# Performance work log

Hardware: AMD Instinct MI355X
Metric: run time of the kernel (lower is better)

## Reference

```python
import jax, jax.numpy as jnp
import numpy as np
from jax import lax

C, NORI, NROT, K, PAD = 256, 8, 2, 3, 1
B, H, W = 16, 64, 64
EPS = 1e-5


def setup_inputs() -> dict:
    key = jax.random.key(0)
    k1, k2, k3 = jax.random.split(key, 3)
    x = jax.random.normal(k1, (B, C, H, W), dtype=jnp.float32)
    # rotate_arf() output: [nRot*C, nOri*C, K, K]
    weight_all = jax.random.normal(k2, (NROT * C, NORI * C, K, K), dtype=jnp.float32) * 0.02
    bias_all = jax.random.normal(k3, (NROT * C,), dtype=jnp.float32) * 0.02
    alpha = jnp.float32(1.0)
    gamma = jnp.ones((C,), dtype=jnp.float32)
    beta = jnp.zeros((C,), dtype=jnp.float32)
    return {"x": x, "weight_all": weight_all, "bias_all": bias_all,
            "alpha": alpha, "gamma": gamma, "beta": beta}


def _forward(x, weight_all, bias_all, alpha, gamma, beta):
    # Loop of nOri*nRot convs over the same x with different weight blocks,
    # all accumulated into one [B,C,H,W] tensor == single conv with summed blocks
    # (conv is linear in the weights): fused form of the original loop.
    W_eff = weight_all.reshape(NROT, C, NORI, C, K, K).sum(axis=(0, 2))  # [C, C, K, K]
    b_eff = bias_all.reshape(NROT, C).sum(axis=0) * NORI                 # [C]
    d_sum = lax.conv_general_dilated(
        x, W_eff, window_strides=(1, 1), padding=[(PAD, PAD), (PAD, PAD)],
        dimension_numbers=("NCHW", "OIHW", "NCHW"))
    d_sum = d_sum + b_eff[None, :, None, None]
    d_mean = d_sum / float(NORI * NROT)
    out = x + alpha * d_mean
    # BatchNorm2d, training mode: biased batch stats over (B, H, W)
    mean = out.mean(axis=(0, 2, 3))
    var = ((out - mean[None, :, None, None]) ** 2).mean(axis=(0, 2, 3))
    inv = lax.rsqrt(var + EPS)
    y = (out - mean[None, :, None, None]) * (gamma * inv)[None, :, None, None] \
        + beta[None, :, None, None]
    return y


def reference(x, weight_all, bias_all, alpha, gamma, beta):
    return _forward(x, weight_all, bias_all, alpha, gamma, beta)
```

## Files before the change

kernel.cpp:

```cpp
#include <hip/hip_runtime.h>
#include <stdint.h>

typedef __attribute__((__ext_vector_type__(8))) __bf16 bf16x8;
typedef __attribute__((__ext_vector_type__(4))) float  f32x4;

#define XT_OFF    0ul
#define WT_OFF    33554432ul
#define BEFF_OFF  34734080ul
#define ZERO_OFF  34737152ul
#define STATS_OFF 34737408ul

__device__ inline void gload_lds16(const void* g, void* l) {
  __builtin_amdgcn_global_load_lds((const __attribute__((address_space(1))) void*)g,
                                   (__attribute__((address_space(3))) void*)l,
                                   16, 0, 0);
}

__global__ void k_wred(const float* __restrict__ w, const float* __restrict__ bias,
                       const float* __restrict__ alpha_p, __bf16* __restrict__ Wt,
                       float* __restrict__ beff, float* __restrict__ zerob,
                       float* __restrict__ statsG) {
  const int co = blockIdx.x;
  const int ci = threadIdx.x;
  float a[9];
#pragma unroll
  for (int t = 0; t < 9; ++t) a[t] = 0.f;
#pragma unroll
  for (int r = 0; r < 2; ++r)
#pragma unroll
    for (int o = 0; o < 8; ++o) {
      const float* p = w + ((size_t)(r * 256 + co) * 2048 + (size_t)(o * 256 + ci)) * 9;
#pragma unroll
      for (int t = 0; t < 9; ++t) a[t] += p[t];
    }
  const float sc = alpha_p[0] * 0.0625f;
#pragma unroll
  for (int t = 0; t < 9; ++t)
    Wt[((size_t)co * 9 + t) * 256 + ci] = (__bf16)(a[t] * sc);
  if (ci == 0) beff[co] = (bias[co] + bias[256 + co]) * 8.0f * sc;
  if (blockIdx.x == 0) {
    statsG[ci] = 0.f; statsG[256 + ci] = 0.f;
    if (ci < 64) zerob[ci] = 0.f;
  }
}

__global__ void k_xpose(const float* __restrict__ x, __bf16* __restrict__ xT) {
  __shared__ __bf16 lds[64 * 258];
  int bh = blockIdx.x;
  int b = bh >> 6, h = bh & 63;
  int t = threadIdx.x;
  int w = t & 63, cg = t >> 6;
  const float* xb = x + ((size_t)b * 16384 + h) * 64;
#pragma unroll 4
  for (int cb = 0; cb < 256; cb += 4) {
    int ci = cb + cg;
    lds[w * 258 + ci] = (__bf16)xb[(size_t)ci * 4096 + w];
  }
  __syncthreads();
  const uint32_t* l32 = (const uint32_t*)lds;
  uint32_t* o32 = (uint32_t*)(xT + ((size_t)b * 64 + h) * 64 * 256);
  int c2 = t & 127, wg = t >> 7;
  for (int w0 = 0; w0 < 64; w0 += 2) {
    int ww = w0 + wg;
    o32[ww * 128 + c2] = l32[ww * 129 + c2];
  }
}

#define A_BYTES 51200
#define B_BYTES 32768

__global__ __launch_bounds__(1024) void k_conv(
    const float* __restrict__ x, const __bf16* __restrict__ xT,
    const __bf16* __restrict__ Wt, const float* __restrict__ beff,
    const __bf16* __restrict__ zerob, float* __restrict__ out,
    float* __restrict__ statsG)
{
  __shared__ __align__(16) char lds[A_BYTES + 2 * B_BYTES];
  const int bb   = blockIdx.x >> 4;
  const int ho0  = (blockIdx.x & 15) << 2;
  const int tid  = threadIdx.x;
  const int lane = tid & 63;
  const int wid  = tid >> 6;
  const int wr   = wid >> 2;
  const int wc   = wid & 3;

  f32x4 acc[4][4];
#pragma unroll
  for (int i = 0; i < 4; ++i)
#pragma unroll
    for (int j = 0; j < 4; ++j)
#pragma unroll
      for (int r = 0; r < 4; ++r) acc[i][j][r] = 0.f;

  const char* zb = (const char*)zerob;

  int boff[4][2];
#pragma unroll
  for (int j = 0; j < 4; ++j)
#pragma unroll
    for (int kk = 0; kk < 2; ++kk) {
      const int co     = (wc << 6) + (j << 4) + (lane & 15);
      const int ci_off = (kk << 5) + ((lane >> 4) << 3);
      boff[j][kk] = ((co << 7) + (ci_off << 1)) ^ ((co & 7) << 4);
    }
  const int bl = lane >> 3;
  const size_t bsrcLane = (size_t)bl * 4608 + (size_t)(((lane & 7) ^ (bl & 7)) << 4);

  auto stageA = [&](int s) {
    const int ci0 = s << 6;
    for (int t = wid; t < 50; t += 16) {
      const int ch = (t << 3) + (lane >> 3);
      const int r  = ch / 66;
      const int c  = ch - r * 66;
      const int ir = ho0 - 1 + r;
      const int ic = c - 1;
      const int k  = (lane & 7) ^ (ch & 7);
      const char* src;
      if (ch < 396 && ir >= 0 && ir < 64 && ic >= 0 && ic < 64)
        src = (const char*)(xT + ((((size_t)bb << 6) + ir) * 64 + ic) * 256 + ci0 + (k << 3));
      else
        src = zb + (k << 4);
      gload_lds16(src, lds + (t << 10));
    }
  };

  auto stageB = [&](int bi, int phOff ) {
    char* buf = lds + A_BYTES + bi * B_BYTES;
    const char* wsrc = (const char*)Wt + bsrcLane + phOff;
    gload_lds16(wsrc + (size_t)wid * 36864, buf + (wid << 10));
    gload_lds16(wsrc + (size_t)(wid + 16) * 36864, buf + ((wid + 16) << 10));
  };

  stageA(0);
  stageB(0, 0);
  __syncthreads();

  int pb = 0;
  for (int s = 0; s < 4; ++s) {
    for (int tap = 0; tap < 9; ++tap) {
      const int p = s * 9 + tap;
      if (p + 1 < 36) {
        int ntap = tap + 1, ns = s;
        if (ntap == 9) { ntap = 0; ++ns; }
        stageB(pb ^ 1, ((ntap << 8) + (ns << 6)) << 1);
      }
      const int dh = (tap >= 6) ? 2 : (tap >= 3 ? 1 : 0);
      const int dw = tap - dh * 3;
      const char* Bb = lds + A_BYTES + pb * B_BYTES;
      __builtin_amdgcn_s_setprio(1);
#pragma unroll
      for (int kk = 0; kk < 2; ++kk) {
        const int ci_off = (kk << 5) + ((lane >> 4) << 3);
        bf16x8 av[4];
#pragma unroll
        for (int i = 0; i < 4; ++i) {
          const int pos = (wr + dh) * 66 + (i << 4) + (lane & 15) + dw;
          const int off = ((pos << 7) + (ci_off << 1)) ^ ((pos & 7) << 4);
          av[i] = *(const bf16x8*)(lds + off);
        }
#pragma unroll
        for (int j = 0; j < 4; ++j) {
          const bf16x8 bv = *(const bf16x8*)(Bb + boff[j][kk]);
#pragma unroll
          for (int i = 0; i < 4; ++i)
            acc[i][j] = __builtin_amdgcn_mfma_f32_16x16x32_bf16(av[i], bv, acc[i][j], 0, 0, 0);
        }
      }
      __builtin_amdgcn_s_setprio(0);
      __syncthreads();
      if (tap == 8 && s < 3) {
        stageA(s + 1);
        __syncthreads();
      }
      pb ^= 1;
    }
  }

  __syncthreads();
  float* sw    = (float*)lds + wid * 1040;
  float* lstat = (float*)(lds + 112640);
  if (tid < 512) lstat[tid] = 0.f;
  __syncthreads();

  const int cl = lane & 15, ch4 = (lane >> 4) << 2;
  const int ho = ho0 + wr;
  const int cc2 = lane >> 2, q = lane & 3;
#pragma unroll
  for (int j = 0; j < 4; ++j) {
    asm volatile("s_waitcnt lgkmcnt(0)" ::: "memory");
#pragma unroll
    for (int i = 0; i < 4; ++i)
#pragma unroll
      for (int r = 0; r < 4; ++r)
        sw[cl * 65 + (i << 4) + ch4 + r] = acc[i][j][r];
    asm volatile("s_waitcnt lgkmcnt(0)" ::: "memory");
    for (int cc = 0; cc < 16; ++cc) {
      const int co = (wc << 6) + (j << 4) + cc;
      const float conv = sw[cc * 65 + lane];
      const size_t oi = ((((size_t)bb << 8) + (size_t)co) << 12) + (ho << 6) + lane;
      const float v = x[oi] + conv + beff[co];
      out[oi] = v;
      sw[cc * 65 + lane] = v;
    }
    asm volatile("s_waitcnt lgkmcnt(0)" ::: "memory");
    float r1 = 0.f, r2 = 0.f;
#pragma unroll
    for (int k = 0; k < 16; ++k) {
      const float vv = sw[cc2 * 65 + (q << 4) + k];
      r1 += vv; r2 += vv * vv;
    }
    r1 += __shfl_xor(r1, 1); r2 += __shfl_xor(r2, 1);
    r1 += __shfl_xor(r1, 2); r2 += __shfl_xor(r2, 2);
    if (q == 0) {
      const int co = (wc << 6) + (j << 4) + cc2;
      atomicAdd(&lstat[co], r1);
      atomicAdd(&lstat[256 + co], r2);
    }
    asm volatile("s_waitcnt lgkmcnt(0)" ::: "memory");
  }
  __syncthreads();
  if (tid < 512) atomicAdd(&statsG[tid], lstat[tid]);
}

__global__ void k_apply(float* __restrict__ out, const float* __restrict__ statsG,
                        const float* __restrict__ gamma, const float* __restrict__ beta) {
  size_t i = (size_t)blockIdx.x * 256 + threadIdx.x;
  int co = (int)((i >> 10) & 255);
  const float mean = statsG[co] * (1.f / 65536.f);
  const float var  = statsG[256 + co] * (1.f / 65536.f) - mean * mean;
  const float inv  = rsqrtf(var + 1e-5f);
  const float sc   = gamma[co] * inv;
  const float sh   = beta[co] - mean * sc;
  float4* p = (float4*)out;
  float4 v = p[i];
  v.x = v.x * sc + sh; v.y = v.y * sc + sh; v.z = v.z * sc + sh; v.w = v.w * sc + sh;
  p[i] = v;
}

extern "C" void kernel_launch(void* const* d_in, const int* in_sizes, int n_in,
                              void* d_out, int out_size, void* d_ws, size_t ws_size,
                              hipStream_t stream) {
  const float* x     = (const float*)d_in[0];
  const float* wall  = (const float*)d_in[1];
  const float* bias  = (const float*)d_in[2];
  const float* alpha = (const float*)d_in[3];
  const float* gamma = (const float*)d_in[4];
  const float* beta  = (const float*)d_in[5];
  float* out = (float*)d_out;

  char* ws = (char*)d_ws;
  __bf16* xT     = (__bf16*)(ws + XT_OFF);
  __bf16* Wt     = (__bf16*)(ws + WT_OFF);
  float*  beff   = (float*)(ws + BEFF_OFF);
  float*  zerob  = (float*)(ws + ZERO_OFF);
  float*  statsG = (float*)(ws + STATS_OFF);

  k_wred<<<256, 256, 0, stream>>>(wall, bias, alpha, Wt, beff, zerob, statsG);
  k_xpose<<<1024, 256, 0, stream>>>(x, xT);
  k_conv<<<256, 1024, 0, stream>>>(x, xT, Wt, beff, (const __bf16*)zerob, out, statsG);
  k_apply<<<16384, 256, 0, stream>>>(out, statsG, gamma, beta);
}
```

Measured before the change: 129.0 us.

## Halve conv block threads, double per-wave tile, add triple-buffered weight pipeline

The conv kernel now runs 8 waves per block instead of 16. Each wave computes two output rows (8x4 MFMA tiles), so every B-fragment load from LDS is reused across twice as many MFMAs. Weight staging moves from double to triple buffering. It uses explicit vmcnt waits and raw barriers, which removes the per-tap __syncthreads, and the weight layout is reordered so each phase's tile is contiguous. The cost is higher register pressure from 128 accumulator floats per lane, more LDS, and fewer waves to hide latency, so the vmcnt counting has to be exactly right.

After: 130.9 us. Within noise of the previous version (+1.5%).

```diff
diff --git a/kernel.cpp b/kernel.cpp
--- a/kernel.cpp
+++ b/kernel.cpp
@@ -34,9 +34,10 @@
       for (int t = 0; t < 9; ++t) a[t] += p[t];
     }
   const float sc = alpha_p[0] * 0.0625f;
+  const int s = ci >> 6, cis = ci & 63;
 #pragma unroll
   for (int t = 0; t < 9; ++t)
-    Wt[((size_t)co * 9 + t) * 256 + ci] = (__bf16)(a[t] * sc);
+    Wt[(size_t)(t * 4 + s) * 16384 + co * 64 + cis] = (__bf16)(a[t] * sc);
   if (ci == 0) beff[co] = (bias[co] + bias[256 + co]) * 8.0f * sc;
   if (blockIdx.x == 0) {
     statsG[ci] = 0.f; statsG[256 + ci] = 0.f;
@@ -69,13 +70,13 @@
 #define A_BYTES 51200
 #define B_BYTES 32768
 
-__global__ __launch_bounds__(1024) void k_conv(
+__global__ __launch_bounds__(512) void k_conv(
     const float* __restrict__ x, const __bf16* __restrict__ xT,
     const __bf16* __restrict__ Wt, const float* __restrict__ beff,
     const __bf16* __restrict__ zerob, float* __restrict__ out,
     float* __restrict__ statsG)
 {
-  __shared__ __align__(16) char lds[A_BYTES + 2 * B_BYTES];
+  __shared__ __align__(16) char lds[A_BYTES + 3 * B_BYTES];
   const int bb   = blockIdx.x >> 4;
   const int ho0  = (blockIdx.x & 15) << 2;
   const int tid  = threadIdx.x;
@@ -84,9 +85,9 @@
   const int wr   = wid >> 2;
   const int wc   = wid & 3;
 
-  f32x4 acc[4][4];
-#pragma unroll
-  for (int i = 0; i < 4; ++i)
+  f32x4 acc[8][4];
+#pragma unroll
+  for (int i = 0; i < 8; ++i)
 #pragma unroll
     for (int j = 0; j < 4; ++j)
 #pragma unroll
@@ -104,11 +105,11 @@
       boff[j][kk] = ((co << 7) + (ci_off << 1)) ^ ((co & 7) << 4);
     }
   const int bl = lane >> 3;
-  const size_t bsrcLane = (size_t)bl * 4608 + (size_t)(((lane & 7) ^ (bl & 7)) << 4);
+  const int bsrcLane = (bl << 7) + (((lane & 7) ^ (bl & 7)) << 4);
 
   auto stageA = [&](int s) {
     const int ci0 = s << 6;
-    for (int t = wid; t < 50; t += 16) {
+    for (int t = wid; t < 50; t += 8) {
       const int ch = (t << 3) + (lane >> 3);
       const int r  = ch / 66;
       const int c  = ch - r * 66;
@@ -124,89 +125,99 @@
     }
   };
 
-  auto stageB = [&](int bi, int phOff ) {
-    char* buf = lds + A_BYTES + bi * B_BYTES;
-    const char* wsrc = (const char*)Wt + bsrcLane + phOff;
-    gload_lds16(wsrc + (size_t)wid * 36864, buf + (wid << 10));
-    gload_lds16(wsrc + (size_t)(wid + 16) * 36864, buf + ((wid + 16) << 10));
+  auto stageB = [&](int ph) {
+    char* buf = lds + A_BYTES + (ph % 3) * B_BYTES;
+    const int tap = ph / 4 - (ph / 36) * 9;
+    (void)tap;
+    const int s2 = ph / 9, tp = ph - s2 * 9;
+    const char* wsrc = (const char*)Wt + ((size_t)(tp * 4 + s2) << 15) + bsrcLane;
+#pragma unroll
+    for (int it = 0; it < 4; ++it) {
+      const int t = wid + (it << 3);
+      gload_lds16(wsrc + (t << 10), buf + (t << 10));
+    }
   };
 
   stageA(0);
-  stageB(0, 0);
-  __syncthreads();
-
-  int pb = 0;
-  for (int s = 0; s < 4; ++s) {
-    for (int tap = 0; tap < 9; ++tap) {
-      const int p = s * 9 + tap;
-      if (p + 1 < 36) {
-        int ntap = tap + 1, ns = s;
-        if (ntap == 9) { ntap = 0; ++ns; }
-        stageB(pb ^ 1, ((ntap << 8) + (ns << 6)) << 1);
+  stageB(0);
+  stageB(1);
+  asm volatile("s_waitcnt vmcnt(4)" ::: "memory");
+  __builtin_amdgcn_s_barrier();
+
+  int s = 0, tap = 0;
+  for (int p = 0; p < 36; ++p) {
+    if (p > 0) {
+      if (p == 35) asm volatile("s_waitcnt vmcnt(0)" ::: "memory");
+      else         asm volatile("s_waitcnt vmcnt(4)" ::: "memory");
+      __builtin_amdgcn_s_barrier();
+    }
+    const bool bnd = (tap == 0) && (p > 0);
+    if (bnd) stageA(s);
+    if (p + 2 < 36) stageB(p + 2);
+    if (bnd) asm volatile("s_waitcnt vmcnt(4)" ::: "memory");
+
+    const int dh = (tap >= 6) ? 2 : (tap >= 3 ? 1 : 0);
+    const int dw = tap - dh * 3;
+    const char* Bb = lds + A_BYTES + (p % 3) * B_BYTES;
+    __builtin_amdgcn_s_setprio(1);
+#pragma unroll
+    for (int kk = 0; kk < 2; ++kk) {
+      const int ci_off = (kk << 5) + ((lane >> 4) << 3);
+      bf16x8 av[8];
+#pragma unroll
+      for (int i = 0; i < 8; ++i) {
+        const int pos = ((wr << 1) + (i >> 2) + dh) * 66 + ((i & 3) << 4) + (lane & 15) + dw;
+        const int off = ((pos << 7) + (ci_off << 1)) ^ ((pos & 7) << 4);
+        av[i] = *(const bf16x8*)(lds + off);
       }
-      const int dh = (tap >= 6) ? 2 : (tap >= 3 ? 1 : 0);
-      const int dw = tap - dh * 3;
-      const char* Bb = lds + A_BYTES + pb * B_BYTES;
-      __builtin_amdgcn_s_setprio(1);
-#pragma unroll
-      for (int kk = 0; kk < 2; ++kk) {
-        const int ci_off = (kk << 5) + ((lane >> 4) << 3);
-        bf16x8 av[4];
-#pragma unroll
-        for (int i = 0; i < 4; ++i) {
-          const int pos = (wr + dh) * 66 + (i << 4) + (lane & 15) + dw;
-          const int off = ((pos << 7) + (ci_off << 1)) ^ ((pos & 7) << 4);
-          av[i] = *(const bf16x8*)(lds + off);
-        }
-#pragma unroll
-        for (int j = 0; j < 4; ++j) {
-          const bf16x8 bv = *(const bf16x8*)(Bb + boff[j][kk]);
-#pragma unroll
-          for (int i = 0; i < 4; ++i)
-            acc[i][j] = __builtin_amdgcn_mfma_f32_16x16x32_bf16(av[i], bv, acc[i][j], 0, 0, 0);
-        }
+#pragma unroll
+      for (int j = 0; j < 4; ++j) {
+        const bf16x8 bv = *(const bf16x8*)(Bb + boff[j][kk]);
+#pragma unroll
+        for (int i = 0; i < 8; ++i)
+          acc[i][j] = __builtin_amdgcn_mfma_f32_16x16x32_bf16(av[i], bv, acc[i][j], 0, 0, 0);
       }
-      __builtin_amdgcn_s_setprio(0);
-      __syncthreads();
-      if (tap == 8 && s < 3) {
-        stageA(s + 1);
-        __syncthreads();
-      }
-      pb ^= 1;
-    }
-  }
-
-  __syncthreads();
-  float* sw    = (float*)lds + wid * 1040;
-  float* lstat = (float*)(lds + 112640);
+    }
+    __builtin_amdgcn_s_setprio(0);
+
+    if (++tap == 9) { tap = 0; ++s; }
+  }
+
+  __syncthreads();
+  float* sw    = (float*)lds + wid * 2064;
+  float* lstat = (float*)(lds + 131072);
   if (tid < 512) lstat[tid] = 0.f;
   __syncthreads();
 
   const int cl = lane & 15, ch4 = (lane >> 4) << 2;
-  const int ho = ho0 + wr;
   const int cc2 = lane >> 2, q = lane & 3;
 #pragma unroll
   for (int j = 0; j < 4; ++j) {
     asm volatile("s_waitcnt lgkmcnt(0)" ::: "memory");
 #pragma unroll
-    for (int i = 0; i < 4; ++i)
+    for (int i = 0; i < 8; ++i)
 #pragma unroll
       for (int r = 0; r < 4; ++r)
-        sw[cl * 65 + (i << 4) + ch4 + r] = acc[i][j][r];
+        sw[cl * 129 + (i << 4) + ch4 + r] = acc[i][j][r];
     asm volatile("s_waitcnt lgkmcnt(0)" ::: "memory");
     for (int cc = 0; cc < 16; ++cc) {
       const int co = (wc << 6) + (j << 4) + cc;
-      const float conv = sw[cc * 65 + lane];
-      const size_t oi = ((((size_t)bb << 8) + (size_t)co) << 12) + (ho << 6) + lane;
-      const float v = x[oi] + conv + beff[co];
-      out[oi] = v;
-      sw[cc * 65 + lane] = v;
+      const float be = beff[co];
+#pragma unroll
+      for (int half = 0; half < 2; ++half) {
+        const float conv = sw[cc * 129 + (half << 6) + lane];
+        const int ho = ho0 + (wr << 1) + half;
+        const size_t oi = ((((size_t)bb << 8) + (size_t)co) << 12) + (ho << 6) + lane;
+        const float v = x[oi] + conv + be;
+        out[oi] = v;
+        sw[cc * 129 + (half << 6) + lane] = v;
+      }
     }
     asm volatile("s_waitcnt lgkmcnt(0)" ::: "memory");
     float r1 = 0.f, r2 = 0.f;
 #pragma unroll
-    for (int k = 0; k < 16; ++k) {
-      const float vv = sw[cc2 * 65 + (q << 4) + k];
+    for (int k = 0; k < 32; ++k) {
+      const float vv = sw[cc2 * 129 + (q << 5) + k];
       r1 += vv; r2 += vv * vv;
     }
     r1 += __shfl_xor(r1, 1); r2 += __shfl_xor(r2, 1);
@@ -257,6 +268,6 @@
 
   k_wred<<<256, 256, 0, stream>>>(wall, bias, alpha, Wt, beff, zerob, statsG);
   k_xpose<<<1024, 256, 0, stream>>>(x, xT);
-  k_conv<<<256, 1024, 0, stream>>>(x, xT, Wt, beff, (const __bf16*)zerob, out, statsG);
+  k_conv<<<256, 512, 0, stream>>>(x, xT, Wt, beff, (const __bf16*)zerob, out, statsG);
   k_apply<<<16384, 256, 0, stream>>>(out, statsG, gamma, beta);
 }
```

## Fuse BN apply into conv via cooperative grid sync; merge prep kernels

Applied to the files above, without the earlier changes.

Merges the weight-reduction and transpose kernels into one launch, and rearranges the reduced weight layout so each stage's B tile is a contiguous 32KB block. The conv kernel now keeps the pre-norm outputs in registers, performs a cooperative grid-wide sync after the statistics atomics, then applies the batch-norm scale and shift and writes the output once. This drops the separate apply kernel, which read and rewrote the whole output. The cost is a grid barrier and the requirement that all 256 blocks of 1024 threads be co-resident.

Result: slower. 169.9 us (+31.8%).

```diff
diff --git a/kernel.cpp b/kernel.cpp
--- a/kernel.cpp
+++ b/kernel.cpp
@@ -1,4 +1,5 @@
 #include <hip/hip_runtime.h>
+#include <hip/hip_cooperative_groups.h>
 #include <stdint.h>
 
 typedef __attribute__((__ext_vector_type__(8))) __bf16 bf16x8;
@@ -16,53 +17,55 @@
                                    16, 0, 0);
 }
 
-__global__ void k_wred(const float* __restrict__ w, const float* __restrict__ bias,
+__global__ void k_prep(const float* __restrict__ w, const float* __restrict__ bias,
                        const float* __restrict__ alpha_p, __bf16* __restrict__ Wt,
                        float* __restrict__ beff, float* __restrict__ zerob,
-                       float* __restrict__ statsG) {
-  const int co = blockIdx.x;
-  const int ci = threadIdx.x;
-  float a[9];
-#pragma unroll
-  for (int t = 0; t < 9; ++t) a[t] = 0.f;
-#pragma unroll
-  for (int r = 0; r < 2; ++r)
-#pragma unroll
-    for (int o = 0; o < 8; ++o) {
-      const float* p = w + ((size_t)(r * 256 + co) * 2048 + (size_t)(o * 256 + ci)) * 9;
-#pragma unroll
-      for (int t = 0; t < 9; ++t) a[t] += p[t];
-    }
-  const float sc = alpha_p[0] * 0.0625f;
-#pragma unroll
-  for (int t = 0; t < 9; ++t)
-    Wt[((size_t)co * 9 + t) * 256 + ci] = (__bf16)(a[t] * sc);
-  if (ci == 0) beff[co] = (bias[co] + bias[256 + co]) * 8.0f * sc;
-  if (blockIdx.x == 0) {
-    statsG[ci] = 0.f; statsG[256 + ci] = 0.f;
-    if (ci < 64) zerob[ci] = 0.f;
-  }
-}
-
-__global__ void k_xpose(const float* __restrict__ x, __bf16* __restrict__ xT) {
+                       float* __restrict__ statsG,
+                       const float* __restrict__ x, __bf16* __restrict__ xT) {
   __shared__ __bf16 lds[64 * 258];
-  int bh = blockIdx.x;
-  int b = bh >> 6, h = bh & 63;
-  int t = threadIdx.x;
-  int w = t & 63, cg = t >> 6;
-  const float* xb = x + ((size_t)b * 16384 + h) * 64;
+  if (blockIdx.x < 256) {
+    const int co = blockIdx.x;
+    const int ci = threadIdx.x;
+    float a[9];
+#pragma unroll
+    for (int t = 0; t < 9; ++t) a[t] = 0.f;
+#pragma unroll
+    for (int r = 0; r < 2; ++r)
+#pragma unroll
+      for (int o = 0; o < 8; ++o) {
+        const float* p = w + ((size_t)(r * 256 + co) * 2048 + (size_t)(o * 256 + ci)) * 9;
+#pragma unroll
+        for (int t = 0; t < 9; ++t) a[t] += p[t];
+      }
+    const float sc = alpha_p[0] * 0.0625f;
+    const int s = ci >> 6, cis = ci & 63;
+#pragma unroll
+    for (int t = 0; t < 9; ++t)
+      Wt[(size_t)(t * 4 + s) * 16384 + co * 64 + cis] = (__bf16)(a[t] * sc);
+    if (ci == 0) beff[co] = (bias[co] + bias[256 + co]) * 8.0f * sc;
+    if (blockIdx.x == 0) {
+      statsG[ci] = 0.f; statsG[256 + ci] = 0.f;
+      if (ci < 64) zerob[ci] = 0.f;
+    }
+  } else {
+    int bh = blockIdx.x - 256;
+    int b = bh >> 6, h = bh & 63;
+    int t = threadIdx.x;
+    int w2 = t & 63, cg = t >> 6;
+    const float* xb = x + ((size_t)b * 16384 + h) * 64;
 #pragma unroll 4
-  for (int cb = 0; cb < 256; cb += 4) {
-    int ci = cb + cg;
-    lds[w * 258 + ci] = (__bf16)xb[(size_t)ci * 4096 + w];
-  }
-  __syncthreads();
-  const uint32_t* l32 = (const uint32_t*)lds;
-  uint32_t* o32 = (uint32_t*)(xT + ((size_t)b * 64 + h) * 64 * 256);
-  int c2 = t & 127, wg = t >> 7;
-  for (int w0 = 0; w0 < 64; w0 += 2) {
-    int ww = w0 + wg;
-    o32[ww * 128 + c2] = l32[ww * 129 + c2];
+    for (int cb = 0; cb < 256; cb += 4) {
+      int ci = cb + cg;
+      lds[w2 * 258 + ci] = (__bf16)xb[(size_t)ci * 4096 + w2];
+    }
+    __syncthreads();
+    const uint32_t* l32 = (const uint32_t*)lds;
+    uint32_t* o32 = (uint32_t*)(xT + ((size_t)b * 64 + h) * 64 * 256);
+    int c2 = t & 127, wg = t >> 7;
+    for (int w0 = 0; w0 < 64; w0 += 2) {
+      int ww = w0 + wg;
+      o32[ww * 128 + c2] = l32[ww * 129 + c2];
+    }
   }
 }
 
@@ -73,7 +76,8 @@
     const float* __restrict__ x, const __bf16* __restrict__ xT,
     const __bf16* __restrict__ Wt, const float* __restrict__ beff,
     const __bf16* __restrict__ zerob, float* __restrict__ out,
-    float* __restrict__ statsG)
+    float* __restrict__ statsG, const float* __restrict__ gamma,
+    const float* __restrict__ beta)
 {
   __shared__ __align__(16) char lds[A_BYTES + 2 * B_BYTES];
   const int bb   = blockIdx.x >> 4;
@@ -104,7 +108,7 @@
       boff[j][kk] = ((co << 7) + (ci_off << 1)) ^ ((co & 7) << 4);
     }
   const int bl = lane >> 3;
-  const size_t bsrcLane = (size_t)bl * 4608 + (size_t)(((lane & 7) ^ (bl & 7)) << 4);
+  const int bsrcLane = (bl << 7) + (((lane & 7) ^ (bl & 7)) << 4);
 
   auto stageA = [&](int s) {
     const int ci0 = s << 6;
@@ -124,15 +128,15 @@
     }
   };
 
-  auto stageB = [&](int bi, int phOff ) {
+  auto stageB = [&](int bi, int s2, int tp) {
     char* buf = lds + A_BYTES + bi * B_BYTES;
-    const char* wsrc = (const char*)Wt + bsrcLane + phOff;
-    gload_lds16(wsrc + (size_t)wid * 36864, buf + (wid << 10));
-    gload_lds16(wsrc + (size_t)(wid + 16) * 36864, buf + ((wid + 16) << 10));
+    const char* wsrc = (const char*)Wt + ((size_t)(tp * 4 + s2) << 15) + bsrcLane;
+    gload_lds16(wsrc + (wid << 10), buf + (wid << 10));
+    gload_lds16(wsrc + ((wid + 16) << 10), buf + ((wid + 16) << 10));
   };
 
   stageA(0);
-  stageB(0, 0);
+  stageB(0, 0, 0);
   __syncthreads();
 
   int pb = 0;
@@ -142,7 +146,7 @@
       if (p + 1 < 36) {
         int ntap = tap + 1, ns = s;
         if (ntap == 9) { ntap = 0; ++ns; }
-        stageB(pb ^ 1, ((ntap << 8) + (ns << 6)) << 1);
+        stageB(pb ^ 1, ns, ntap);
       }
       const int dh = (tap >= 6) ? 2 : (tap >= 3 ? 1 : 0);
       const int dw = tap - dh * 3;
@@ -184,34 +188,34 @@
 
   const int cl = lane & 15, ch4 = (lane >> 4) << 2;
   const int ho = ho0 + wr;
-  const int cc2 = lane >> 2, q = lane & 3;
+  const int cc2 = lane >> 2, q2 = lane & 3;
 #pragma unroll
   for (int j = 0; j < 4; ++j) {
-    asm volatile("s_waitcnt lgkmcnt(0)" ::: "memory");
 #pragma unroll
     for (int i = 0; i < 4; ++i)
 #pragma unroll
       for (int r = 0; r < 4; ++r)
         sw[cl * 65 + (i << 4) + ch4 + r] = acc[i][j][r];
     asm volatile("s_waitcnt lgkmcnt(0)" ::: "memory");
+#pragma unroll
     for (int cc = 0; cc < 16; ++cc) {
       const int co = (wc << 6) + (j << 4) + cc;
       const float conv = sw[cc * 65 + lane];
       const size_t oi = ((((size_t)bb << 8) + (size_t)co) << 12) + (ho << 6) + lane;
       const float v = x[oi] + conv + beff[co];
-      out[oi] = v;
+      acc[cc >> 2][j][cc & 3] = v;
       sw[cc * 65 + lane] = v;
     }
     asm volatile("s_waitcnt lgkmcnt(0)" ::: "memory");
     float r1 = 0.f, r2 = 0.f;
 #pragma unroll
     for (int k = 0; k < 16; ++k) {
-      const float vv = sw[cc2 * 65 + (q << 4) + k];
+      const float vv = sw[cc2 * 65 + (q2 << 4) + k];
       r1 += vv; r2 += vv * vv;
     }
     r1 += __shfl_xor(r1, 1); r2 += __shfl_xor(r2, 1);
     r1 += __shfl_xor(r1, 2); r2 += __shfl_xor(r2, 2);
-    if (q == 0) {
+    if (q2 == 0) {
       const int co = (wc << 6) + (j << 4) + cc2;
       atomicAdd(&lstat[co], r1);
       atomicAdd(&lstat[256 + co], r2);
@@ -220,21 +224,27 @@
   }
   __syncthreads();
   if (tid < 512) atomicAdd(&statsG[tid], lstat[tid]);
-}
-
-__global__ void k_apply(float* __restrict__ out, const float* __restrict__ statsG,
-                        const float* __restrict__ gamma, const float* __restrict__ beta) {
-  size_t i = (size_t)blockIdx.x * 256 + threadIdx.x;
-  int co = (int)((i >> 10) & 255);
-  const float mean = statsG[co] * (1.f / 65536.f);
-  const float var  = statsG[256 + co] * (1.f / 65536.f) - mean * mean;
-  const float inv  = rsqrtf(var + 1e-5f);
-  const float sc   = gamma[co] * inv;
-  const float sh   = beta[co] - mean * sc;
-  float4* p = (float4*)out;
-  float4 v = p[i];
-  v.x = v.x * sc + sh; v.y = v.y * sc + sh; v.z = v.z * sc + sh; v.w = v.w * sc + sh;
-  p[i] = v;
+
+  cooperative_groups::this_grid().sync();
+
+  if (tid < 256) {
+    const float mean = statsG[tid] * (1.f / 65536.f);
+    const float var  = statsG[256 + tid] * (1.f / 65536.f) - mean * mean;
+    const float inv  = rsqrtf(var + 1e-5f);
+    const float sc   = gamma[tid] * inv;
+    lstat[tid]       = sc;
+    lstat[256 + tid] = beta[tid] - mean * sc;
+  }
+  __syncthreads();
+#pragma unroll
+  for (int j = 0; j < 4; ++j) {
+#pragma unroll
+    for (int cc = 0; cc < 16; ++cc) {
+      const int co = (wc << 6) + (j << 4) + cc;
+      const size_t oi = ((((size_t)bb << 8) + (size_t)co) << 12) + (ho << 6) + lane;
+      out[oi] = acc[cc >> 2][j][cc & 3] * lstat[co] + lstat[256 + co];
+    }
+  }
 }
 
 extern "C" void kernel_launch(void* const* d_in, const int* in_sizes, int n_in,
@@ -255,8 +265,15 @@
   float*  zerob  = (float*)(ws + ZERO_OFF);
   float*  statsG = (float*)(ws + STATS_OFF);
 
-  k_wred<<<256, 256, 0, stream>>>(wall, bias, alpha, Wt, beff, zerob, statsG);
-  k_xpose<<<1024, 256, 0, stream>>>(x, xT);
-  k_conv<<<256, 1024, 0, stream>>>(x, xT, Wt, beff, (const __bf16*)zerob, out, statsG);
-  k_apply<<<16384, 256, 0, stream>>>(out, statsG, gamma, beta);
-}
+  k_prep<<<1280, 256, 0, stream>>>(wall, bias, alpha, Wt, beff, zerob, statsG, x, xT);
+
+  const __bf16* xTc = xT;
+  const __bf16* Wtc = Wt;
+  const float*  beffc = beff;
+  const __bf16* zbc = (const __bf16*)zerob;
+  void* args[] = {(void*)&x, (void*)&xTc, (void*)&Wtc, (void*)&beffc,
+                  (void*)&zbc, (void*)&out, (void*)&statsG,
+                  (void*)&gamma, (void*)&beta};
+  hipLaunchCooperativeKernel((const void*)k_conv, dim3(256), dim3(1024),
+                             args, 0, stream);
+}
```

## Triple-buffer weight tiles, relayout weights contiguously, and write conv epilogue directly

Applied to the files above, without the earlier changes.

Weights are stored per (tap, channel-slice) as contiguous 32KB tiles, so each weight-stage load is one contiguous block rather than a strided gather. The weight pipeline goes from double to triple buffering: loads run two phases ahead, and barriers wait on vmcnt(2) instead of a full sync each step. The epilogue drops the LDS transpose and writes float4 output straight from accumulator registers, reducing batch-norm statistics with shuffles. This uses more LDS per block and depends on careful counting of outstanding loads.

New measurement: 127.4 us. About the same (-1.2%).

```diff
diff --git a/kernel.cpp b/kernel.cpp
--- a/kernel.cpp
+++ b/kernel.cpp
@@ -34,9 +34,10 @@
       for (int t = 0; t < 9; ++t) a[t] += p[t];
     }
   const float sc = alpha_p[0] * 0.0625f;
+  const int s = ci >> 6, cis = ci & 63;
 #pragma unroll
   for (int t = 0; t < 9; ++t)
-    Wt[((size_t)co * 9 + t) * 256 + ci] = (__bf16)(a[t] * sc);
+    Wt[(size_t)(t * 4 + s) * 16384 + co * 64 + cis] = (__bf16)(a[t] * sc);
   if (ci == 0) beff[co] = (bias[co] + bias[256 + co]) * 8.0f * sc;
   if (blockIdx.x == 0) {
     statsG[ci] = 0.f; statsG[256 + ci] = 0.f;
@@ -75,7 +76,7 @@
     const __bf16* __restrict__ zerob, float* __restrict__ out,
     float* __restrict__ statsG)
 {
-  __shared__ __align__(16) char lds[A_BYTES + 2 * B_BYTES];
+  __shared__ __align__(16) char lds[A_BYTES + 3 * B_BYTES + 2048];
   const int bb   = blockIdx.x >> 4;
   const int ho0  = (blockIdx.x & 15) << 2;
   const int tid  = threadIdx.x;
@@ -83,6 +84,7 @@
   const int wid  = tid >> 6;
   const int wr   = wid >> 2;
   const int wc   = wid & 3;
+  const int l15  = lane & 15;
 
   f32x4 acc[4][4];
 #pragma unroll
@@ -99,12 +101,12 @@
   for (int j = 0; j < 4; ++j)
 #pragma unroll
     for (int kk = 0; kk < 2; ++kk) {
-      const int co     = (wc << 6) + (j << 4) + (lane & 15);
+      const int co     = (wc << 6) + (j << 4) + l15;
       const int ci_off = (kk << 5) + ((lane >> 4) << 3);
       boff[j][kk] = ((co << 7) + (ci_off << 1)) ^ ((co & 7) << 4);
     }
   const int bl = lane >> 3;
-  const size_t bsrcLane = (size_t)bl * 4608 + (size_t)(((lane & 7) ^ (bl & 7)) << 4);
+  const int bsrcLane = (bl << 7) + (((lane & 7) ^ (bl & 7)) << 4);
 
   auto stageA = [&](int s) {
     const int ci0 = s << 6;
@@ -124,99 +126,104 @@
     }
   };
 
-  auto stageB = [&](int bi, int phOff ) {
+  auto stageB = [&](int ph, int bi) {
     char* buf = lds + A_BYTES + bi * B_BYTES;
-    const char* wsrc = (const char*)Wt + bsrcLane + phOff;
-    gload_lds16(wsrc + (size_t)wid * 36864, buf + (wid << 10));
-    gload_lds16(wsrc + (size_t)(wid + 16) * 36864, buf + ((wid + 16) << 10));
+    const int s2 = ph / 9, tp = ph - s2 * 9;
+    const char* wsrc = (const char*)Wt + ((size_t)(tp * 4 + s2) << 15) + bsrcLane;
+    gload_lds16(wsrc + (wid << 10), buf + (wid << 10));
+    gload_lds16(wsrc + ((wid + 16) << 10), buf + ((wid + 16) << 10));
   };
 
   stageA(0);
   stageB(0, 0);
-  __syncthreads();
-
-  int pb = 0;
-  for (int s = 0; s < 4; ++s) {
-    for (int tap = 0; tap < 9; ++tap) {
-      const int p = s * 9 + tap;
-      if (p + 1 < 36) {
-        int ntap = tap + 1, ns = s;
-        if (ntap == 9) { ntap = 0; ++ns; }
-        stageB(pb ^ 1, ((ntap << 8) + (ns << 6)) << 1);
+  stageB(1, 1);
+  asm volatile("s_waitcnt vmcnt(0)" ::: "memory");
+  __builtin_amdgcn_s_barrier();
+  asm volatile("" ::: "memory");
+
+  int s = 0, tap = 0, bcur = 0;
+  for (int p = 0; p < 36; ++p) {
+    if (p + 2 < 36) {
+      int bnx = bcur + 2; if (bnx >= 3) bnx -= 3;
+      stageB(p + 2, bnx);
+    }
+    const int dh = (tap >= 6) ? 2 : (tap >= 3 ? 1 : 0);
+    const int dw = tap - dh * 3;
+    const char* Bb = lds + A_BYTES + bcur * B_BYTES;
+    __builtin_amdgcn_s_setprio(1);
+#pragma unroll
+    for (int kk = 0; kk < 2; ++kk) {
+      const int ci_off = (kk << 5) + ((lane >> 4) << 3);
+      bf16x8 av[4];
+#pragma unroll
+      for (int i = 0; i < 4; ++i) {
+        const int pos = (wr + dh) * 66 + (i << 4) + l15 + dw;
+        const int off = ((pos << 7) + (ci_off << 1)) ^ ((pos & 7) << 4);
+        av[i] = *(const bf16x8*)(lds + off);
       }
-      const int dh = (tap >= 6) ? 2 : (tap >= 3 ? 1 : 0);
-      const int dw = tap - dh * 3;
-      const char* Bb = lds + A_BYTES + pb * B_BYTES;
-      __builtin_amdgcn_s_setprio(1);
-#pragma unroll
-      for (int kk = 0; kk < 2; ++kk) {
-        const int ci_off = (kk << 5) + ((lane >> 4) << 3);
-        bf16x8 av[4];
-#pragma unroll
-        for (int i = 0; i < 4; ++i) {
-          const int pos = (wr + dh) * 66 + (i << 4) + (lane & 15) + dw;
-          const int off = ((pos << 7) + (ci_off << 1)) ^ ((pos & 7) << 4);
-          av[i] = *(const bf16x8*)(lds + off);
-        }
-#pragma unroll
-        for (int j = 0; j < 4; ++j) {
-          const bf16x8 bv = *(const bf16x8*)(Bb + boff[j][kk]);
-#pragma unroll
-          for (int i = 0; i < 4; ++i)
-            acc[i][j] = __builtin_amdgcn_mfma_f32_16x16x32_bf16(av[i], bv, acc[i][j], 0, 0, 0);
-        }
+#pragma unroll
+      for (int j = 0; j < 4; ++j) {
+        const bf16x8 bv = *(const bf16x8*)(Bb + boff[j][kk]);
+#pragma unroll
+        for (int i = 0; i < 4; ++i)
+          acc[i][j] = __builtin_amdgcn_mfma_f32_16x16x32_bf16(av[i], bv, acc[i][j], 0, 0, 0);
       }
-      __builtin_amdgcn_s_setprio(0);
-      __syncthreads();
-      if (tap == 8 && s < 3) {
-        stageA(s + 1);
-        __syncthreads();
-      }
-      pb ^= 1;
-    }
-  }
-
-  __syncthreads();
-  float* sw    = (float*)lds + wid * 1040;
-  float* lstat = (float*)(lds + 112640);
+    }
+    __builtin_amdgcn_s_setprio(0);
+
+    if (tap == 8 && s < 3) {
+      asm volatile("s_waitcnt vmcnt(0)" ::: "memory");
+      __builtin_amdgcn_s_barrier();
+      asm volatile("" ::: "memory");
+      stageA(s + 1);
+      asm volatile("s_waitcnt vmcnt(0)" ::: "memory");
+      __builtin_amdgcn_s_barrier();
+      asm volatile("" ::: "memory");
+    } else if (p + 2 < 36) {
+      asm volatile("s_waitcnt vmcnt(2)" ::: "memory");
+      __builtin_amdgcn_s_barrier();
+      asm volatile("" ::: "memory");
+    } else if (p < 35) {
+      asm volatile("s_waitcnt vmcnt(0)" ::: "memory");
+      __builtin_amdgcn_s_barrier();
+      asm volatile("" ::: "memory");
+    }
+    if (++tap == 9) { tap = 0; ++s; }
+    if (++bcur == 3) bcur = 0;
+  }
+
+  __syncthreads();
+  float* lstat = (float*)(lds + A_BYTES + 3 * B_BYTES);
   if (tid < 512) lstat[tid] = 0.f;
   __syncthreads();
 
-  const int cl = lane & 15, ch4 = (lane >> 4) << 2;
+  const int wq = lane >> 4;
   const int ho = ho0 + wr;
-  const int cc2 = lane >> 2, q = lane & 3;
 #pragma unroll
   for (int j = 0; j < 4; ++j) {
-    asm volatile("s_waitcnt lgkmcnt(0)" ::: "memory");
-#pragma unroll
-    for (int i = 0; i < 4; ++i)
-#pragma unroll
-      for (int r = 0; r < 4; ++r)
-        sw[cl * 65 + (i << 4) + ch4 + r] = acc[i][j][r];
-    asm volatile("s_waitcnt lgkmcnt(0)" ::: "memory");
-    for (int cc = 0; cc < 16; ++cc) {
-      const int co = (wc << 6) + (j << 4) + cc;
-      const float conv = sw[cc * 65 + lane];
-      const size_t oi = ((((size_t)bb << 8) + (size_t)co) << 12) + (ho << 6) + lane;
-      const float v = x[oi] + conv + beff[co];
-      out[oi] = v;
-      sw[cc * 65 + lane] = v;
-    }
-    asm volatile("s_waitcnt lgkmcnt(0)" ::: "memory");
+    const int co = (wc << 6) + (j << 4) + l15;
+    const float be = beff[co];
+    const size_t base = ((((size_t)bb << 8) + (size_t)co) << 12) + (ho << 6);
     float r1 = 0.f, r2 = 0.f;
 #pragma unroll
-    for (int k = 0; k < 16; ++k) {
-      const float vv = sw[cc2 * 65 + (q << 4) + k];
-      r1 += vv; r2 += vv * vv;
-    }
-    r1 += __shfl_xor(r1, 1); r2 += __shfl_xor(r2, 1);
-    r1 += __shfl_xor(r1, 2); r2 += __shfl_xor(r2, 2);
-    if (q == 0) {
-      const int co = (wc << 6) + (j << 4) + cc2;
+    for (int i = 0; i < 4; ++i) {
+      const int w0 = (i << 4) + (wq << 2);
+      const float4 xv = *(const float4*)(x + base + w0);
+      float4 v;
+      v.x = acc[i][j][0] + xv.x + be;
+      v.y = acc[i][j][1] + xv.y + be;
+      v.z = acc[i][j][2] + xv.z + be;
+      v.w = acc[i][j][3] + xv.w + be;
+      r1 += v.x + v.y + v.z + v.w;
+      r2 += v.x * v.x + v.y * v.y + v.z * v.z + v.w * v.w;
+      *(float4*)(out + base + w0) = v;
+    }
+    r1 += __shfl_xor(r1, 16); r2 += __shfl_xor(r2, 16);
+    r1 += __shfl_xor(r1, 32); r2 += __shfl_xor(r2, 32);
+    if (lane < 16) {
       atomicAdd(&lstat[co], r1);
       atomicAdd(&lstat[256 + co], r2);
     }
-    asm volatile("s_waitcnt lgkmcnt(0)" ::: "memory");
   }
   __syncthreads();
   if (tid < 512) atomicAdd(&statsG[tid], lstat[tid]);
```
